# Performance work log

Measured on AMD Instinct MI355X. Metric: run time of the kernel, lower is better.

The kernel has to match this reference:

```python
import jax, jax.numpy as jnp
import numpy as np

B, N, D = 4, 2048, 512

def setup_inputs() -> dict:
    key = jax.random.key(0)
    ks = jax.random.split(key, 7)
    s = 1.0 / np.sqrt(D)
    return {
        "x": jax.random.normal(ks[0], (B, N, D), dtype=jnp.float32),
        "Wq": jax.random.uniform(ks[1], (D, D), jnp.float32, -s, s),
        "bq": jax.random.uniform(ks[2], (D,), jnp.float32, -s, s),
        "Wk": jax.random.uniform(ks[3], (D, D), jnp.float32, -s, s),
        "bk": jax.random.uniform(ks[4], (D,), jnp.float32, -s, s),
        "Wv": jax.random.uniform(ks[5], (D, D), jnp.float32, -s, s),
        "bv": jax.random.uniform(ks[6], (D,), jnp.float32, -s, s),
    }

def reference(x, Wq, bq, Wk, bk, Wv, bv):
    # QKV projections (torch Linear: y = x @ W^T + b)
    q = jnp.einsum('bnd,ed->bne', x, Wq) + bq
    k = jnp.einsum('bnd,ed->bne', x, Wk) + bk
    v = jnp.einsum('bnd,ed->bne', x, Wv) + bv
    scale = 1.0 / jnp.sqrt(jnp.asarray(q.shape[-1], q.dtype))
    scores = jnp.einsum('bqd,bkd->bqk', q, k) * scale  # [B,N,N]
    weights = jax.nn.softmax(scores, axis=-1)
    return jnp.einsum('bqk,bkd->bqd', weights, v)
```

## Files before the change

### kernel.cpp

```cpp
#include <hip/hip_runtime.h>
#include <cstdint>
#include <cstddef>

#define BATCH 4
#define SEQ 2048
#define DIM 512

using floatx4 = __attribute__((ext_vector_type(4))) float;
using shortx8 = __attribute__((ext_vector_type(8))) short;
using halfx8  = __attribute__((ext_vector_type(8))) _Float16;

__device__ __forceinline__ ushort f2bf(float f) {
    union { float f; uint32_t u; } v; v.f = f;
    uint32_t r = v.u + 0x7FFFu + ((v.u >> 16) & 1u);
    return (ushort)(r >> 16);
}
__device__ __forceinline__ ushort f2h(float f) {
    _Float16 h = (_Float16)f;
    return __builtin_bit_cast(unsigned short, h);
}

__global__ void prep_k(const float* __restrict__ x,
                       const float* __restrict__ Wq, const float* __restrict__ Wk,
                       const float* __restrict__ Wv,
                       const float* __restrict__ bq, const float* __restrict__ bk,
                       const float* __restrict__ bv,
                       ushort* __restrict__ xb, ushort* __restrict__ wcat,
                       float* __restrict__ bcat) {
    int i = blockIdx.x * 256 + threadIdx.x;
    if (i < 1048576) {
        float4 v = ((const float4*)x)[i];
        ((ushort4*)xb)[i] = make_ushort4(f2bf(v.x), f2bf(v.y), f2bf(v.z), f2bf(v.w));
    } else if (i < 1048576 + 196608) {
        int j = i - 1048576;
        int which = j >> 16;
        const float* w = (which == 0) ? Wq : (which == 1) ? Wk : Wv;
        float4 v = ((const float4*)w)[j & 0xFFFF];
        ((ushort4*)wcat)[j] = make_ushort4(f2bf(v.x), f2bf(v.y), f2bf(v.z), f2bf(v.w));
    } else if (i < 1048576 + 196608 + 384) {
        int j = i - 1245184;
        const float* bsrc = (j < 128) ? bq : (j < 256) ? bk : bv;
        ((float4*)bcat)[j] = ((const float4*)bsrc)[j & 127];
    }
}

__global__ void transpose_v_k(const ushort* __restrict__ qkv, ushort* __restrict__ vt) {
    __shared__ ushort t[32][33];
    int b  = blockIdx.z;
    int j0 = blockIdx.x * 32;
    int e0 = blockIdx.y * 32;
    for (int r = threadIdx.y; r < 32; r += 8)
        t[r][threadIdx.x] = qkv[(size_t)(b * SEQ + j0 + r) * 1536 + 1024 + e0 + threadIdx.x];
    __syncthreads();
    for (int r = threadIdx.y; r < 32; r += 8)
        vt[((size_t)b * DIM + e0 + r) * SEQ + j0 + threadIdx.x] = t[threadIdx.x][r];
}


template<int EPI, bool F16>
__global__ __launch_bounds__(256, 2)
void gemm_k(const ushort* __restrict__ A, const ushort* __restrict__ B,
            void* __restrict__ Cout, const float* __restrict__ bias,
            float* __restrict__ rowsum,
            int lda, int ldb, int ldc, int kIters, float alpha,
            long sA, long sB, long sC)
{
    __shared__ __align__(16) ushort As[2][128 * 32];
    __shared__ __align__(16) ushort Bs[2][128 * 32];
    __shared__ float rsum[128];

    const int tid = threadIdx.x;
    const int bz = blockIdx.z;
    int b, kofs, slab;
    if (EPI == 2) { b = bz >> 1; kofs = (bz & 1) << 10; slab = ((bz & 1) << 2) + b; }
    else          { b = bz; kofs = 0; slab = bz; }
    const ushort* Ab = A + (size_t)b * sA + kofs;
    const ushort* Bb = B + (size_t)b * sB + kofs;

    const int m0 = blockIdx.y * 128;
    const int n0 = blockIdx.x * 128;
    const int lane = tid & 63, wave = tid >> 6;
    const int wm = (wave >> 1) * 64, wn = (wave & 1) * 64;
    const int quad = lane >> 4, l16 = lane & 15;
    const int swz = (l16 >> 1) & 3;

    const int s0 = tid, s1 = tid + 256;
    const int r0 = s0 >> 2, r1 = s1 >> 2;
    const int kc0 = (s0 & 3) ^ ((r0 >> 1) & 3);
    const int kc1 = (s1 & 3) ^ ((r1 >> 1) & 3);
    const ushort* gA0 = Ab + (size_t)(m0 + r0) * lda + kc0 * 8;
    const ushort* gA1 = Ab + (size_t)(m0 + r1) * lda + kc1 * 8;
    const ushort* gB0 = Bb + (size_t)(n0 + r0) * ldb + kc0 * 8;
    const ushort* gB1 = Bb + (size_t)(n0 + r1) * ldb + kc1 * 8;

#define STAGE(kk, bufi) do {                                                              \
    int ko = (kk) * 32;                                                                   \
    __builtin_amdgcn_global_load_lds((const __attribute__((address_space(1))) uint32_t*)(gA0 + ko), \
        (__attribute__((address_space(3))) uint32_t*)(&As[bufi][s0 * 8]), 16, 0, 0);      \
    __builtin_amdgcn_global_load_lds((const __attribute__((address_space(1))) uint32_t*)(gA1 + ko), \
        (__attribute__((address_space(3))) uint32_t*)(&As[bufi][s1 * 8]), 16, 0, 0);      \
    __builtin_amdgcn_global_load_lds((const __attribute__((address_space(1))) uint32_t*)(gB0 + ko), \
        (__attribute__((address_space(3))) uint32_t*)(&Bs[bufi][s0 * 8]), 16, 0, 0);      \
    __builtin_amdgcn_global_load_lds((const __attribute__((address_space(1))) uint32_t*)(gB1 + ko), \
        (__attribute__((address_space(3))) uint32_t*)(&Bs[bufi][s1 * 8]), 16, 0, 0);      \
} while (0)

    int ofsA[4], ofsB[4];
#pragma unroll
    for (int mi = 0; mi < 4; mi++)
        ofsA[mi] = ((wm + mi * 16 + l16) * 4 + (quad ^ swz)) * 8;
#pragma unroll
    for (int ni = 0; ni < 4; ni++)
        ofsB[ni] = ((wn + ni * 16 + l16) * 4 + (quad ^ swz)) * 8;

    floatx4 acc[4][4];
#pragma unroll
    for (int i = 0; i < 4; i++)
#pragma unroll
        for (int j = 0; j < 4; j++)
            acc[i][j] = (floatx4){0.f, 0.f, 0.f, 0.f};

    if (EPI == 1 && tid < 128) rsum[tid] = 0.f;

    STAGE(0, 0);
    for (int it = 0; it < kIters; ++it) {
        __syncthreads();
        const int buf = it & 1;
        if (it + 1 < kIters) STAGE(it + 1, buf ^ 1);
        if constexpr (F16) {
            halfx8 af[4], bfr[4];
#pragma unroll
            for (int mi = 0; mi < 4; mi++) af[mi] = *(const halfx8*)&As[buf][ofsA[mi]];
#pragma unroll
            for (int ni = 0; ni < 4; ni++) bfr[ni] = *(const halfx8*)&Bs[buf][ofsB[ni]];
#pragma unroll
            for (int mi = 0; mi < 4; mi++)
#pragma unroll
                for (int ni = 0; ni < 4; ni++)
                    acc[mi][ni] = __builtin_amdgcn_mfma_f32_16x16x32_f16(af[mi], bfr[ni], acc[mi][ni], 0, 0, 0);
        } else {
            shortx8 af[4], bfr[4];
#pragma unroll
            for (int mi = 0; mi < 4; mi++) af[mi] = *(const shortx8*)&As[buf][ofsA[mi]];
#pragma unroll
            for (int ni = 0; ni < 4; ni++) bfr[ni] = *(const shortx8*)&Bs[buf][ofsB[ni]];
#pragma unroll
            for (int mi = 0; mi < 4; mi++)
#pragma unroll
                for (int ni = 0; ni < 4; ni++)
                    acc[mi][ni] = __builtin_amdgcn_mfma_f32_16x16x32_bf16(af[mi], bfr[ni], acc[mi][ni], 0, 0, 0);
        }
    }
#undef STAGE

    if constexpr (EPI == 0) {
        float bvv[4];
#pragma unroll
        for (int ni = 0; ni < 4; ni++) bvv[ni] = bias[n0 + wn + ni * 16 + l16];
#pragma unroll
        for (int mi = 0; mi < 4; mi++) {
#pragma unroll
            for (int ni = 0; ni < 4; ni++) {
                int col = n0 + wn + ni * 16 + l16;
#pragma unroll
                for (int r = 0; r < 4; r++) {
                    int row = m0 + wm + mi * 16 + quad * 4 + r;
                    float v = acc[mi][ni][r] + bvv[ni];
                    ((ushort*)Cout)[(size_t)row * ldc + col] = (col < 1024) ? f2bf(v) : f2h(v);
                }
            }
        }
    } else if constexpr (EPI == 1) {
#pragma unroll
        for (int mi = 0; mi < 4; mi++) {
#pragma unroll
            for (int r = 0; r < 4; r++) {
                int rl = wm + mi * 16 + quad * 4 + r;
                float ps = 0.f;
#pragma unroll
                for (int ni = 0; ni < 4; ni++) {
                    int col = n0 + wn + ni * 16 + l16;
                    float e = __expf(acc[mi][ni][r] * alpha);
                    ((ushort*)Cout)[(size_t)slab * sC + (size_t)(m0 + rl) * ldc + col] = f2h(e);
                    ps += e;
                }
                atomicAdd(&rsum[rl], ps);
            }
        }
        __syncthreads();
        if (tid < 128) atomicAdd(&rowsum[b * SEQ + m0 + tid], rsum[tid]);
    } else {
#pragma unroll
        for (int mi = 0; mi < 4; mi++) {
#pragma unroll
            for (int ni = 0; ni < 4; ni++) {
                int col = n0 + wn + ni * 16 + l16;
#pragma unroll
                for (int r = 0; r < 4; r++) {
                    int row = m0 + wm + mi * 16 + quad * 4 + r;
                    ((float*)Cout)[(size_t)slab * sC + (size_t)row * ldc + col] = acc[mi][ni][r];
                }
            }
        }
    }
}

__global__ void reduce_scale_k(const float* __restrict__ part, const float* __restrict__ rowsum,
                               float* __restrict__ out) {
    int i = blockIdx.x * 256 + threadIdx.x;
    float4 a = ((const float4*)part)[i];
    float4 c = ((const float4*)(part + 4LL * SEQ * DIM))[i];
    float inv = 1.0f / rowsum[i >> 7];
    float4 o;
    o.x = (a.x + c.x) * inv;
    o.y = (a.y + c.y) * inv;
    o.z = (a.z + c.z) * inv;
    o.w = (a.w + c.w) * inv;
    ((float4*)out)[i] = o;
}

extern "C" void kernel_launch(void* const* d_in, const int* in_sizes, int n_in,
                              void* d_out, int out_size, void* d_ws, size_t ws_size,
                              hipStream_t stream) {
    const float* x  = (const float*)d_in[0];
    const float* Wq = (const float*)d_in[1];
    const float* bq = (const float*)d_in[2];
    const float* Wk = (const float*)d_in[3];
    const float* bk = (const float*)d_in[4];
    const float* Wv = (const float*)d_in[5];
    const float* bv = (const float*)d_in[6];
    float* out = (float*)d_out;
    char* ws = (char*)d_ws;

    ushort* xb      = (ushort*)(ws);
    ushort* wcat    = (ushort*)(ws + 8388608);
    float*  bcat    = (float* )(ws + 9961472);
    ushort* qkvb    = (ushort*)(ws + 9967616);
    ushort* vt      = (ushort*)(ws + 35133440);
    ushort* Pb      = (ushort*)(ws + 43522048);
    float*  rowsum  = (float* )(ws + 77076480);
    float*  partial = (float* )(ws + 77109248);

    hipMemsetAsync(rowsum, 0, 8192 * 4, stream);

    prep_k<<<4866, 256, 0, stream>>>(x, Wq, Wk, Wv, bq, bk, bv, xb, wcat, bcat);

    gemm_k<0, false><<<dim3(12, 64, 1), 256, 0, stream>>>(
        xb, wcat, qkvb, bcat, nullptr, 512, 512, 1536, 16, 1.0f, 0, 0, 0);

    transpose_v_k<<<dim3(64, 16, 4), dim3(32, 8), 0, stream>>>(qkvb, vt);

    const float scale = 0.04419417382415922f;
    gemm_k<1, false><<<dim3(16, 16, 4), 256, 0, stream>>>(
        qkvb, qkvb + 512, Pb, nullptr, rowsum, 1536, 1536, 2048, 16, scale,
        (long)SEQ * 1536, (long)SEQ * 1536, (long)SEQ * SEQ);

    gemm_k<2, true><<<dim3(4, 16, 8), 256, 0, stream>>>(
        Pb, vt, partial, nullptr, nullptr, 2048, 2048, 512, 32, 1.0f,
        (long)SEQ * SEQ, (long)DIM * SEQ, (long)SEQ * DIM);

    reduce_scale_k<<<4096, 256, 0, stream>>>(partial, rowsum, out);
}
```

Baseline: 199.0 us.

## Fuse V transpose into projection epilogue, switch to fp16, stage outputs via LDS

The QKV projection epilogue now writes V transposed directly, so the separate transpose kernel goes away. All GEMMs move from bf16 to fp16, and the Q/K and P epilogues are staged through swizzled shared memory so global stores are coalesced 16-byte writes. The P·V split-K goes from 2 to 4 slices with higher occupancy (launch bounds 3), and the final reduce sums 4 partials. The gains come from fewer launches, coalesced stores and better occupancy. The cost is a larger partial buffer and more reduction traffic, plus an extra LDS round trip in the epilogue.

```diff
diff --git a/kernel.cpp b/kernel.cpp
--- a/kernel.cpp
+++ b/kernel.cpp
@@ -2,19 +2,12 @@
 #include <cstdint>
 #include <cstddef>
 
-#define BATCH 4
 #define SEQ 2048
 #define DIM 512
 
 using floatx4 = __attribute__((ext_vector_type(4))) float;
-using shortx8 = __attribute__((ext_vector_type(8))) short;
 using halfx8  = __attribute__((ext_vector_type(8))) _Float16;
 
-__device__ __forceinline__ ushort f2bf(float f) {
-    union { float f; uint32_t u; } v; v.f = f;
-    uint32_t r = v.u + 0x7FFFu + ((v.u >> 16) & 1u);
-    return (ushort)(r >> 16);
-}
 __device__ __forceinline__ ushort f2h(float f) {
     _Float16 h = (_Float16)f;
     return __builtin_bit_cast(unsigned short, h);
@@ -25,18 +18,18 @@
                        const float* __restrict__ Wv,
                        const float* __restrict__ bq, const float* __restrict__ bk,
                        const float* __restrict__ bv,
-                       ushort* __restrict__ xb, ushort* __restrict__ wcat,
+                       ushort* __restrict__ xh, ushort* __restrict__ wcat,
                        float* __restrict__ bcat) {
     int i = blockIdx.x * 256 + threadIdx.x;
     if (i < 1048576) {
         float4 v = ((const float4*)x)[i];
-        ((ushort4*)xb)[i] = make_ushort4(f2bf(v.x), f2bf(v.y), f2bf(v.z), f2bf(v.w));
+        ((ushort4*)xh)[i] = make_ushort4(f2h(v.x), f2h(v.y), f2h(v.z), f2h(v.w));
     } else if (i < 1048576 + 196608) {
         int j = i - 1048576;
         int which = j >> 16;
         const float* w = (which == 0) ? Wq : (which == 1) ? Wk : Wv;
         float4 v = ((const float4*)w)[j & 0xFFFF];
-        ((ushort4*)wcat)[j] = make_ushort4(f2bf(v.x), f2bf(v.y), f2bf(v.z), f2bf(v.w));
+        ((ushort4*)wcat)[j] = make_ushort4(f2h(v.x), f2h(v.y), f2h(v.z), f2h(v.w));
     } else if (i < 1048576 + 196608 + 384) {
         int j = i - 1245184;
         const float* bsrc = (j < 128) ? bq : (j < 256) ? bk : bv;
@@ -44,36 +37,24 @@
     }
 }
 
-__global__ void transpose_v_k(const ushort* __restrict__ qkv, ushort* __restrict__ vt) {
-    __shared__ ushort t[32][33];
-    int b  = blockIdx.z;
-    int j0 = blockIdx.x * 32;
-    int e0 = blockIdx.y * 32;
-    for (int r = threadIdx.y; r < 32; r += 8)
-        t[r][threadIdx.x] = qkv[(size_t)(b * SEQ + j0 + r) * 1536 + 1024 + e0 + threadIdx.x];
-    __syncthreads();
-    for (int r = threadIdx.y; r < 32; r += 8)
-        vt[((size_t)b * DIM + e0 + r) * SEQ + j0 + threadIdx.x] = t[threadIdx.x][r];
-}
-
-
-template<int EPI, bool F16>
-__global__ __launch_bounds__(256, 2)
+
+template<int EPI>
+__global__ __launch_bounds__(256, 3)
 void gemm_k(const ushort* __restrict__ A, const ushort* __restrict__ B,
             void* __restrict__ Cout, const float* __restrict__ bias,
-            float* __restrict__ rowsum,
+            float* __restrict__ rowsum, ushort* __restrict__ vt,
             int lda, int ldb, int ldc, int kIters, float alpha,
             long sA, long sB, long sC)
 {
-    __shared__ __align__(16) ushort As[2][128 * 32];
-    __shared__ __align__(16) ushort Bs[2][128 * 32];
+    __shared__ __align__(16) ushort smem[2][2][4096];
     __shared__ float rsum[128];
+    ushort* Ps = &smem[0][0][0];
 
     const int tid = threadIdx.x;
     const int bz = blockIdx.z;
-    int b, kofs, slab;
-    if (EPI == 2) { b = bz >> 1; kofs = (bz & 1) << 10; slab = ((bz & 1) << 2) + b; }
-    else          { b = bz; kofs = 0; slab = bz; }
+    int b, kofs;
+    if (EPI == 2) { b = bz & 3; kofs = (bz >> 2) * 512; }
+    else          { b = bz; kofs = 0; }
     const ushort* Ab = A + (size_t)b * sA + kofs;
     const ushort* Bb = B + (size_t)b * sB + kofs;
 
@@ -96,13 +77,13 @@
 #define STAGE(kk, bufi) do {                                                              \
     int ko = (kk) * 32;                                                                   \
     __builtin_amdgcn_global_load_lds((const __attribute__((address_space(1))) uint32_t*)(gA0 + ko), \
-        (__attribute__((address_space(3))) uint32_t*)(&As[bufi][s0 * 8]), 16, 0, 0);      \
+        (__attribute__((address_space(3))) uint32_t*)(&smem[0][bufi][s0 * 8]), 16, 0, 0); \
     __builtin_amdgcn_global_load_lds((const __attribute__((address_space(1))) uint32_t*)(gA1 + ko), \
-        (__attribute__((address_space(3))) uint32_t*)(&As[bufi][s1 * 8]), 16, 0, 0);      \
+        (__attribute__((address_space(3))) uint32_t*)(&smem[0][bufi][s1 * 8]), 16, 0, 0); \
     __builtin_amdgcn_global_load_lds((const __attribute__((address_space(1))) uint32_t*)(gB0 + ko), \
-        (__attribute__((address_space(3))) uint32_t*)(&Bs[bufi][s0 * 8]), 16, 0, 0);      \
+        (__attribute__((address_space(3))) uint32_t*)(&smem[1][bufi][s0 * 8]), 16, 0, 0); \
     __builtin_amdgcn_global_load_lds((const __attribute__((address_space(1))) uint32_t*)(gB1 + ko), \
-        (__attribute__((address_space(3))) uint32_t*)(&Bs[bufi][s1 * 8]), 16, 0, 0);      \
+        (__attribute__((address_space(3))) uint32_t*)(&smem[1][bufi][s1 * 8]), 16, 0, 0); \
 } while (0)
 
     int ofsA[4], ofsB[4];
@@ -127,80 +108,87 @@
         __syncthreads();
         const int buf = it & 1;
         if (it + 1 < kIters) STAGE(it + 1, buf ^ 1);
-        if constexpr (F16) {
-            halfx8 af[4], bfr[4];
-#pragma unroll
-            for (int mi = 0; mi < 4; mi++) af[mi] = *(const halfx8*)&As[buf][ofsA[mi]];
-#pragma unroll
-            for (int ni = 0; ni < 4; ni++) bfr[ni] = *(const halfx8*)&Bs[buf][ofsB[ni]];
-#pragma unroll
-            for (int mi = 0; mi < 4; mi++)
-#pragma unroll
-                for (int ni = 0; ni < 4; ni++)
-                    acc[mi][ni] = __builtin_amdgcn_mfma_f32_16x16x32_f16(af[mi], bfr[ni], acc[mi][ni], 0, 0, 0);
-        } else {
-            shortx8 af[4], bfr[4];
-#pragma unroll
-            for (int mi = 0; mi < 4; mi++) af[mi] = *(const shortx8*)&As[buf][ofsA[mi]];
-#pragma unroll
-            for (int ni = 0; ni < 4; ni++) bfr[ni] = *(const shortx8*)&Bs[buf][ofsB[ni]];
-#pragma unroll
-            for (int mi = 0; mi < 4; mi++)
-#pragma unroll
-                for (int ni = 0; ni < 4; ni++)
-                    acc[mi][ni] = __builtin_amdgcn_mfma_f32_16x16x32_bf16(af[mi], bfr[ni], acc[mi][ni], 0, 0, 0);
-        }
+        halfx8 af[4], bfr[4];
+#pragma unroll
+        for (int mi = 0; mi < 4; mi++) af[mi] = *(const halfx8*)&smem[0][buf][ofsA[mi]];
+#pragma unroll
+        for (int ni = 0; ni < 4; ni++) bfr[ni] = *(const halfx8*)&smem[1][buf][ofsB[ni]];
+#pragma unroll
+        for (int mi = 0; mi < 4; mi++)
+#pragma unroll
+            for (int ni = 0; ni < 4; ni++)
+                acc[mi][ni] = __builtin_amdgcn_mfma_f32_16x16x32_f16(af[mi], bfr[ni], acc[mi][ni], 0, 0, 0);
     }
 #undef STAGE
 
-    if constexpr (EPI == 0) {
-        float bvv[4];
-#pragma unroll
-        for (int ni = 0; ni < 4; ni++) bvv[ni] = bias[n0 + wn + ni * 16 + l16];
-#pragma unroll
-        for (int mi = 0; mi < 4; mi++) {
+    if constexpr (EPI == 2) {
+#pragma unroll
+        for (int mi = 0; mi < 4; mi++)
 #pragma unroll
             for (int ni = 0; ni < 4; ni++) {
                 int col = n0 + wn + ni * 16 + l16;
 #pragma unroll
                 for (int r = 0; r < 4; r++) {
                     int row = m0 + wm + mi * 16 + quad * 4 + r;
-                    float v = acc[mi][ni][r] + bvv[ni];
-                    ((ushort*)Cout)[(size_t)row * ldc + col] = (col < 1024) ? f2bf(v) : f2h(v);
+                    ((float*)Cout)[(size_t)bz * sC + (size_t)row * ldc + col] = acc[mi][ni][r];
                 }
             }
-        }
-    } else if constexpr (EPI == 1) {
-#pragma unroll
-        for (int mi = 0; mi < 4; mi++) {
-#pragma unroll
-            for (int r = 0; r < 4; r++) {
-                int rl = wm + mi * 16 + quad * 4 + r;
-                float ps = 0.f;
-#pragma unroll
-                for (int ni = 0; ni < 4; ni++) {
-                    int col = n0 + wn + ni * 16 + l16;
-                    float e = __expf(acc[mi][ni][r] * alpha);
-                    ((ushort*)Cout)[(size_t)slab * sC + (size_t)(m0 + rl) * ldc + col] = f2h(e);
-                    ps += e;
+    } else if (EPI == 0 && n0 >= 1024) {
+#pragma unroll
+        for (int ni = 0; ni < 4; ni++) {
+            int col = n0 + wn + ni * 16 + l16;
+            float bv = bias[col];
+            int e = col - 1024;
+#pragma unroll
+            for (int mi = 0; mi < 4; mi++) {
+                int row0 = m0 + wm + mi * 16 + quad * 4;
+                int bb = row0 >> 11;
+                int j = row0 & 2047;
+                ushort4 pk = make_ushort4(f2h(acc[mi][ni][0] + bv), f2h(acc[mi][ni][1] + bv),
+                                          f2h(acc[mi][ni][2] + bv), f2h(acc[mi][ni][3] + bv));
+                *(ushort4*)&vt[((size_t)(bb << 9) + e) * 2048 + j] = pk;
+            }
+        }
+    } else {
+        float bvv[4];
+        if (EPI == 0) {
+#pragma unroll
+            for (int ni = 0; ni < 4; ni++) bvv[ni] = bias[n0 + wn + ni * 16 + l16];
+        }
+        __syncthreads();
+#pragma unroll
+        for (int mi = 0; mi < 4; mi++)
+#pragma unroll
+            for (int ni = 0; ni < 4; ni++) {
+                int col_l = wn + ni * 16 + l16;
+                int c = col_l >> 3, w = col_l & 7;
+#pragma unroll
+                for (int r = 0; r < 4; r++) {
+                    int row_l = wm + mi * 16 + quad * 4 + r;
+                    float v = (EPI == 1) ? __expf(acc[mi][ni][r] * alpha)
+                                         : acc[mi][ni][r] + bvv[ni];
+                    Ps[row_l * 128 + ((c ^ (row_l & 7)) << 3) + w] = f2h(v);
                 }
-                atomicAdd(&rsum[rl], ps);
-            }
-        }
+            }
         __syncthreads();
-        if (tid < 128) atomicAdd(&rowsum[b * SEQ + m0 + tid], rsum[tid]);
-    } else {
-#pragma unroll
-        for (int mi = 0; mi < 4; mi++) {
-#pragma unroll
-            for (int ni = 0; ni < 4; ni++) {
-                int col = n0 + wn + ni * 16 + l16;
-#pragma unroll
-                for (int r = 0; r < 4; r++) {
-                    int row = m0 + wm + mi * 16 + quad * 4 + r;
-                    ((float*)Cout)[(size_t)slab * sC + (size_t)row * ldc + col] = acc[mi][ni][r];
-                }
-            }
+        int rr = tid >> 1, h = tid & 1;
+        float s = 0.f;
+        size_t base = (EPI == 1) ? (size_t)b * sC : 0;
+        ushort* dstrow = (ushort*)Cout + base + (size_t)(m0 + rr) * ldc + n0;
+#pragma unroll
+        for (int j = 0; j < 8; j++) {
+            int c = h * 8 + j;
+            halfx8 p = *(const halfx8*)&Ps[rr * 128 + ((c ^ (rr & 7)) << 3)];
+            if (EPI == 1) {
+#pragma unroll
+                for (int e = 0; e < 8; e++) s += (float)p[e];
+            }
+            *(halfx8*)(dstrow + c * 8) = p;
+        }
+        if (EPI == 1) {
+            atomicAdd(&rsum[rr], s);
+            __syncthreads();
+            if (tid < 128) atomicAdd(&rowsum[b * SEQ + m0 + tid], rsum[tid]);
         }
     }
 }
@@ -208,14 +196,18 @@
 __global__ void reduce_scale_k(const float* __restrict__ part, const float* __restrict__ rowsum,
                                float* __restrict__ out) {
     int i = blockIdx.x * 256 + threadIdx.x;
-    float4 a = ((const float4*)part)[i];
-    float4 c = ((const float4*)(part + 4LL * SEQ * DIM))[i];
-    float inv = 1.0f / rowsum[i >> 7];
-    float4 o;
-    o.x = (a.x + c.x) * inv;
-    o.y = (a.y + c.y) * inv;
-    o.z = (a.z + c.z) * inv;
-    o.w = (a.w + c.w) * inv;
+    int g = i >> 7;
+    int b = g >> 11;
+    int local = i - (b << 18);
+    float4 a = {0.f, 0.f, 0.f, 0.f};
+#pragma unroll
+    for (int kc = 0; kc < 4; kc++) {
+        const float4* p = (const float4*)part + ((size_t)(kc * 4 + b) << 18);
+        float4 v = p[local];
+        a.x += v.x; a.y += v.y; a.z += v.z; a.w += v.w;
+    }
+    float inv = 1.0f / rowsum[g];
+    float4 o = {a.x * inv, a.y * inv, a.z * inv, a.w * inv};
     ((float4*)out)[i] = o;
 }
 
@@ -232,31 +224,28 @@
     float* out = (float*)d_out;
     char* ws = (char*)d_ws;
 
-    ushort* xb      = (ushort*)(ws);
+    float*  partial = (float*)(ws);
+    ushort* xh      = (ushort*)(ws);
     ushort* wcat    = (ushort*)(ws + 8388608);
-    float*  bcat    = (float* )(ws + 9961472);
-    ushort* qkvb    = (ushort*)(ws + 9967616);
-    ushort* vt      = (ushort*)(ws + 35133440);
-    ushort* Pb      = (ushort*)(ws + 43522048);
-    float*  rowsum  = (float* )(ws + 77076480);
-    float*  partial = (float* )(ws + 77109248);
+    float*  bcat    = (float*)(ws + 9961472);
+    float*  rowsum  = (float*)(ws + 67108864);
+    ushort* Pb      = (ushort*)(ws + 67141632);
+    ushort* vt      = (ushort*)(ws + 100696064);
+    ushort* qkh     = (ushort*)(ws + 109084672);
 
     hipMemsetAsync(rowsum, 0, 8192 * 4, stream);
-
-    prep_k<<<4866, 256, 0, stream>>>(x, Wq, Wk, Wv, bq, bk, bv, xb, wcat, bcat);
-
-    gemm_k<0, false><<<dim3(12, 64, 1), 256, 0, stream>>>(
-        xb, wcat, qkvb, bcat, nullptr, 512, 512, 1536, 16, 1.0f, 0, 0, 0);
-
-    transpose_v_k<<<dim3(64, 16, 4), dim3(32, 8), 0, stream>>>(qkvb, vt);
+    prep_k<<<4866, 256, 0, stream>>>(x, Wq, Wk, Wv, bq, bk, bv, xh, wcat, bcat);
+
+    gemm_k<0><<<dim3(12, 64, 1), 256, 0, stream>>>(
+        xh, wcat, qkh, bcat, nullptr, vt, 512, 512, 1024, 16, 1.0f, 0, 0, 0);
 
     const float scale = 0.04419417382415922f;
-    gemm_k<1, false><<<dim3(16, 16, 4), 256, 0, stream>>>(
-        qkvb, qkvb + 512, Pb, nullptr, rowsum, 1536, 1536, 2048, 16, scale,
-        (long)SEQ * 1536, (long)SEQ * 1536, (long)SEQ * SEQ);
-
-    gemm_k<2, true><<<dim3(4, 16, 8), 256, 0, stream>>>(
-        Pb, vt, partial, nullptr, nullptr, 2048, 2048, 512, 32, 1.0f,
+    gemm_k<1><<<dim3(16, 16, 4), 256, 0, stream>>>(
+        qkh, qkh + 512, Pb, nullptr, rowsum, nullptr, 1024, 1024, 2048, 16, scale,
+        (long)SEQ * 1024, (long)SEQ * 1024, (long)SEQ * SEQ);
+
+    gemm_k<2><<<dim3(4, 16, 16), 256, 0, stream>>>(
+        Pb, vt, partial, nullptr, nullptr, nullptr, 2048, 2048, 512, 16, 1.0f,
         (long)SEQ * SEQ, (long)DIM * SEQ, (long)SEQ * DIM);
 
     reduce_scale_k<<<4096, 256, 0, stream>>>(partial, rowsum, out);
```

Result: faster. 190.1 us (-4.5%).
